# Kernel optimization log

Hardware: AMD Instinct MI355X
Metric: run time of the kernel (lower is better)

Reference implementation:

```python
import jax, jax.numpy as jnp
import numpy as np

DEPTH = 4  # truncation depth of the tensor algebra


def _tprod(a, b):
    # tensor (outer) product of level-i and level-j terms, flattened row-major
    # a: (B, C^i), b: (B, C^j) -> (B, C^(i+j))
    return (a[:, :, None] * b[:, None, :]).reshape(a.shape[0], -1)


def _exp_levels(dx):
    # exp(dx) in the truncated tensor algebra: level k = dx^{\otimes k} / k!
    levels = [dx]
    for k in range(2, DEPTH + 1):
        levels.append(_tprod(levels[-1], dx) / k)
    return tuple(levels)


def _chen(a, b):
    # Chen's identity: (a \otimes b)_k = a_k + b_k + sum_{i=1}^{k-1} a_i \otimes b_{k-i}
    out = []
    for k in range(1, DEPTH + 1):
        t = a[k - 1] + b[k - 1]
        for i in range(1, k):
            t = t + _tprod(a[i - 1], b[k - 1 - i])
        out.append(t)
    return tuple(out)


def _log_levels(s):
    # log(1 + x) = sum_{n>=1} (-1)^{n+1}/n x^{\otimes n}, x = S - 1 (levels 1..DEPTH)
    res = list(s)
    power = [t for t in s]  # x^{\otimes 1}; entries may become None (structurally zero)
    for n in range(2, DEPTH + 1):
        new = [None] * DEPTH
        for k in range(n, DEPTH + 1):
            acc = None
            for i in range(n - 1, k):
                if power[i - 1] is None:
                    continue
                term = _tprod(power[i - 1], s[k - i - 1])
                acc = term if acc is None else acc + term
            new[k - 1] = acc
        power = new
        coef = ((-1.0) ** (n + 1)) / n
        for k in range(n, DEPTH + 1):
            if power[k - 1] is not None:
                res[k - 1] = res[k - 1] + coef * power[k - 1]
    return tuple(res)


def _logsignature(path):
    # path: (B, L, C); no basepoint, stream=False, inverse=False, mode='expand'
    dxs = jnp.moveaxis(path[:, 1:] - path[:, :-1], 1, 0)  # (L-1, B, C)
    init = _exp_levels(dxs[0])

    def step(carry, dx):
        return _chen(carry, _exp_levels(dx)), None

    sig, _ = jax.lax.scan(step, init, dxs[1:])
    logsig = _log_levels(sig)
    return jnp.concatenate(logsig, axis=-1)  # (B, C + C^2 + ... + C^DEPTH)


def setup_inputs() -> dict:
    key = jax.random.key(0)
    # scale so high tensor-algebra levels stay well-conditioned in fp32
    path = 0.1 * jax.random.normal(key, (64, 256, 16), dtype=jnp.float32)
    return {"path": path}


def reference(path):
    return _logsignature(path)
```

## Files before the change

### kernel.cpp

```cpp
#include <hip/hip_runtime.h>


#define NC 16
#define NL 256
#define NB 64
#define NSTEP 255
#define OUTB 69904
#define SIG123 4368
#define OFF_L2 16
#define OFF_L3 272
#define OFF_L4 4368

#define SIGA_OFF 0
#define SIGB_OFF (NB * SIG123)
#define B4_OFF (2 * NB * SIG123)

__global__ __launch_bounds__(256, 4) void k_scan(const float* __restrict__ path,
                                                 float* __restrict__ out,
                                                 float* __restrict__ b4,
                                                 float* __restrict__ sigA,
                                                 float* __restrict__ sigB) {
    const int bid = blockIdx.x;
    const int j = bid >> 4;
    const int a = bid & 15;
    const int tid = threadIdx.x;
    const int h = tid >> 7;
    const int b = (tid >> 3) & 15;
    const int c0 = tid & 7;

    __shared__ float Lp[NL * NC];
    __shared__ float Ld[NSTEP * NC];

    const float* pj = path + (size_t)j * NL * NC;
#pragma unroll
    for (int k = 0; k < 4; ++k) {
        const int f = tid + k * 256;
        *(float4*)&Lp[f * 4] = *(const float4*)&pj[f * 4];
    }
    __syncthreads();

#pragma unroll
    for (int k = 0; k < 4; ++k) {
        const int f = tid + k * 256;
        if (f < 1020) {
            const float4 x0 = *(const float4*)&Lp[f * 4];
            const float4 x1 = *(const float4*)&Lp[f * 4 + 16];
            *(float4*)&Ld[f * 4] =
                make_float4(x1.x - x0.x, x1.y - x0.y, x1.z - x0.z, x1.w - x0.w);
        }
    }
    __syncthreads();

    float s4a[16], s4b[16];
#pragma unroll
    for (int d = 0; d < 16; ++d) { s4a[d] = 0.f; s4b[d] = 0.f; }
    float s3_0 = 0.f, s3_1 = 0.f, s2ab = 0.f, s1a = 0.f;

    const int t0 = h ? 128 : 0;
    const int t1 = h ? NSTEP : 128;

    int t = t0;
    const int nv = (t1 - t0) >> 2;
    for (int it = 0; it < nv; ++it) {
#pragma unroll
        for (int u = 0; u < 4; ++u, ++t) {
            const float* r = Ld + t * NC;
            const float4 q0 = *(const float4*)(r);
            const float4 q1 = *(const float4*)(r + 4);
            const float4 q2 = *(const float4*)(r + 8);
            const float4 q3 = *(const float4*)(r + 12);
            const float dxa = r[a];
            const float dxb = r[b];
            const float dxc0 = r[c0];
            const float dxc1 = r[c0 + 8];

            const float P = dxb * s1a;
            const float Q = dxb * dxa;
            const float pre4 = fmaf(1.f / 6.f, P, fmaf(1.f / 24.f, Q, 0.5f * s2ab));
            const float U = fmaf(0.5f, P, fmaf(1.f / 6.f, Q, s2ab));
            const float T0 = fmaf(dxc0, pre4, s3_0);
            const float T1 = fmaf(dxc1, pre4, s3_1);
            const float dv[16] = {q0.x, q0.y, q0.z, q0.w, q1.x, q1.y, q1.z, q1.w,
                                  q2.x, q2.y, q2.z, q2.w, q3.x, q3.y, q3.z, q3.w};
#pragma unroll
            for (int d = 0; d < 16; ++d) {
                s4a[d] = fmaf(dv[d], T0, s4a[d]);
                s4b[d] = fmaf(dv[d], T1, s4b[d]);
            }
            s3_0 = fmaf(dxc0, U, s3_0);
            s3_1 = fmaf(dxc1, U, s3_1);
            s2ab = fmaf(dxb, fmaf(0.5f, dxa, s1a), s2ab);
            s1a += dxa;
        }
    }
    for (; t < t1; ++t) {
        const float* r = Ld + t * NC;
        const float4 q0 = *(const float4*)(r);
        const float4 q1 = *(const float4*)(r + 4);
        const float4 q2 = *(const float4*)(r + 8);
        const float4 q3 = *(const float4*)(r + 12);
        const float dxa = r[a];
        const float dxb = r[b];
        const float dxc0 = r[c0];
        const float dxc1 = r[c0 + 8];
        const float P = dxb * s1a;
        const float Q = dxb * dxa;
        const float pre4 = fmaf(1.f / 6.f, P, fmaf(1.f / 24.f, Q, 0.5f * s2ab));
        const float U = fmaf(0.5f, P, fmaf(1.f / 6.f, Q, s2ab));
        const float T0 = fmaf(dxc0, pre4, s3_0);
        const float T1 = fmaf(dxc1, pre4, s3_1);
        const float dv[16] = {q0.x, q0.y, q0.z, q0.w, q1.x, q1.y, q1.z, q1.w,
                              q2.x, q2.y, q2.z, q2.w, q3.x, q3.y, q3.z, q3.w};
#pragma unroll
        for (int d = 0; d < 16; ++d) {
            s4a[d] = fmaf(dv[d], T0, s4a[d]);
            s4b[d] = fmaf(dv[d], T1, s4b[d]);
        }
        s3_0 = fmaf(dxc0, U, s3_0);
        s3_1 = fmaf(dxc1, U, s3_1);
        s2ab = fmaf(dxb, fmaf(0.5f, dxa, s1a), s2ab);
        s1a += dxa;
    }

    __syncthreads();
    float* ls = Lp;

    if (h == 0) {
        const int base = b * 256 + c0 * 16;
#pragma unroll
        for (int d = 0; d < 16; d += 4) {
            *(float4*)&ls[base + d] = make_float4(s4a[d], s4a[d + 1], s4a[d + 2], s4a[d + 3]);
            *(float4*)&ls[base + 128 + d] =
                make_float4(s4b[d], s4b[d + 1], s4b[d + 2], s4b[d + 3]);
        }
    }
    __syncthreads();
    {
        float* o4 = out + (size_t)j * OUTB + OFF_L4 + a * 4096;
#pragma unroll
        for (int k = 0; k < 4; ++k) {
            const int f = tid + k * 256;
            *(float4*)(o4 + f * 4) = *(const float4*)&ls[f * 4];
        }
    }
    __syncthreads();

    if (h == 1) {
        const int base = b * 256 + c0 * 16;
#pragma unroll
        for (int d = 0; d < 16; d += 4) {
            *(float4*)&ls[base + d] = make_float4(s4a[d], s4a[d + 1], s4a[d + 2], s4a[d + 3]);
            *(float4*)&ls[base + 128 + d] =
                make_float4(s4b[d], s4b[d + 1], s4b[d + 2], s4b[d + 3]);
        }
    }
    __syncthreads();
    {
        float* o4 = b4 + (((size_t)j * 16 + a) << 12);
#pragma unroll
        for (int k = 0; k < 4; ++k) {
            const int f = tid + k * 256;
            *(float4*)(o4 + f * 4) = *(const float4*)&ls[f * 4];
        }
    }

    float* sg = (h ? sigB : sigA) + (size_t)j * SIG123;
    sg[OFF_L3 + (a * 16 + b) * 16 + c0] = s3_0;
    sg[OFF_L3 + (a * 16 + b) * 16 + c0 + 8] = s3_1;
    if (c0 == 0) sg[OFF_L2 + a * 16 + b] = s2ab;
    if ((tid & 127) == 0) sg[a] = s1a;
}

__global__ __launch_bounds__(256) void k_log(const float* __restrict__ sigA,
                                             const float* __restrict__ sigB,
                                             const float* __restrict__ b4,
                                             float* __restrict__ out) {
    const int bid = blockIdx.x;
    const int j = bid >> 4;
    const int a = bid & 15;
    const int tid = threadIdx.x;
    const int q = tid >> 4;
    const int r = tid & 15;

    const float* A = sigA + (size_t)j * SIG123;
    const float* Bp = sigB + (size_t)j * SIG123;

    __shared__ float S1m[16], B1s[16], A2s[16];
    __shared__ float S2m[256], B2s[256], A3s[256];
    __shared__ float S3m[4096], B3s[4096];

    const float b1r = Bp[r];
    const float b2t = Bp[OFF_L2 + tid];

    if (tid < 16) {
        const float bb = Bp[tid];
        B1s[tid] = bb;
        S1m[tid] = A[tid] + bb;
        A2s[tid] = A[OFF_L2 + a * 16 + tid];
    }
    B2s[tid] = b2t;
    S2m[tid] = A[OFF_L2 + tid] + b2t + A[q] * b1r;
    A3s[tid] = A[OFF_L3 + a * 256 + tid];
#pragma unroll
    for (int k = 0; k < 16; ++k) {
        const int m = k * 256 + tid;
        const float b3 = Bp[OFF_L3 + m];
        B3s[m] = b3;
        S3m[m] = A[OFF_L3 + m] + b3 + A[k] * b2t + A[OFF_L2 + k * 16 + q] * b1r;
    }
    __syncthreads();

    const float s1a = S1m[a];
    const float A1a = A[a];
    float* outj = out + (size_t)j * OUTB;
    float* o4 = outj + OFF_L4 + a * 4096;
    const float* B4 = b4 + (((size_t)j * 16 + a) << 12);
    const float Ac = -0.5f * s1a;

#pragma unroll
    for (int k = 0; k < 4; ++k) {
        const int f = tid + k * 256;
        const int m0 = f * 4;
        const int bb = m0 >> 8;
        const int cc = (m0 >> 4) & 15;
        const float s1b = S1m[bb], s1c = S1m[cc];
        const float s2ab = S2m[a * 16 + bb];
        const float s2bc = S2m[bb * 16 + cc];
        const float s3abc = S3m[a * 256 + (m0 >> 4)];
        const float a3x = A3s[m0 >> 4];
        const float a2x = A2s[bb];

        const float4 a4 = *(const float4*)(o4 + m0);
        const float4 b4v = *(const float4*)(B4 + m0);
        const float4 b3v = *(const float4*)(&B3s[m0]);
        const float4 b2v = *(const float4*)(&B2s[m0 & 255]);
        const float4 b1v = *(const float4*)(&B1s[m0 & 15]);
        const float4 v3 = *(const float4*)(&S3m[m0]);
        const float4 v2 = *(const float4*)(&S2m[m0 & 255]);
        const float4 v1 = *(const float4*)(&S1m[m0 & 15]);

        const float Bv = fmaf((1.f / 3.f) * s1a, s1b, -0.5f * s2ab);
        const float Cv = -0.5f * s3abc + (1.f / 3.f) * fmaf(s1a, s2bc, s2ab * s1c)
                         - 0.25f * s1a * s1b * s1c;
        float4 rr;
        rr.x = a4.x + b4v.x + fmaf(A1a, b3v.x, fmaf(a2x, b2v.x, a3x * b1v.x));
        rr.y = a4.y + b4v.y + fmaf(A1a, b3v.y, fmaf(a2x, b2v.y, a3x * b1v.y));
        rr.z = a4.z + b4v.z + fmaf(A1a, b3v.z, fmaf(a2x, b2v.z, a3x * b1v.z));
        rr.w = a4.w + b4v.w + fmaf(A1a, b3v.w, fmaf(a2x, b2v.w, a3x * b1v.w));
        rr.x = fmaf(Ac, v3.x, rr.x) + fmaf(Bv, v2.x, Cv * v1.x);
        rr.y = fmaf(Ac, v3.y, rr.y) + fmaf(Bv, v2.y, Cv * v1.y);
        rr.z = fmaf(Ac, v3.z, rr.z) + fmaf(Bv, v2.z, Cv * v1.z);
        rr.w = fmaf(Ac, v3.w, rr.w) + fmaf(Bv, v2.w, Cv * v1.w);
        *(float4*)(o4 + m0) = rr;
    }

    {
        const float s1b = S1m[q], s1c = S1m[r];
        const float s2ab = S2m[a * 16 + q];
        const float s2bc = S2m[q * 16 + r];
        const float s3abc = S3m[a * 256 + tid];
        const float r3 = s3abc - 0.5f * fmaf(s1a, s2bc, s2ab * s1c)
                         + (1.f / 3.f) * s1a * s1b * s1c;
        outj[OFF_L3 + a * 256 + tid] = r3;
    }
    if (tid < 16) outj[OFF_L2 + a * 16 + tid] = fmaf(-0.5f * s1a, S1m[tid], S2m[a * 16 + tid]);
    if (tid == 0) outj[a] = s1a;
}

extern "C" void kernel_launch(void* const* d_in, const int* in_sizes, int n_in,
                              void* d_out, int out_size, void* d_ws, size_t ws_size,
                              hipStream_t stream) {
    const float* path = (const float*)d_in[0];
    float* out = (float*)d_out;
    float* ws = (float*)d_ws;
    float* sigA = ws + SIGA_OFF;
    float* sigB = ws + SIGB_OFF;
    float* b4 = ws + B4_OFF;

    k_scan<<<NB * 16, 256, 0, stream>>>(path, out, b4, sigA, sigB);
    k_log<<<NB * 16, 256, 0, stream>>>(sigA, sigB, b4, out);
}
```

Before: 113.3 us.

## Merge half-scan level-4 sums in LDS and transpose increments for vector loads

The level-4 partial sums of the two half-scans are now added in shared memory before a single global write, which removes the b4 workspace buffer and its extra global write and read in the log kernel. Path increments are also stored in a channel-major transposed LDS array, so each thread fetches its four scalar channels for four timesteps with one float4 load instead of scalar loads. The log kernel reads B level-3 directly from global memory instead of staging it in shared memory, which lowers LDS use. The cost is an extra barrier and a read-modify-write pass over LDS, plus global loads in the log kernel's inner loop.

After: 109.3 us. -3.5%, faster.

```diff
diff --git a/kernel.cpp b/kernel.cpp
--- a/kernel.cpp
+++ b/kernel.cpp
@@ -13,11 +13,11 @@
 
 #define SIGA_OFF 0
 #define SIGB_OFF (NB * SIG123)
-#define B4_OFF (2 * NB * SIG123)
+
+#define LCS 260
 
 __global__ __launch_bounds__(256, 4) void k_scan(const float* __restrict__ path,
                                                  float* __restrict__ out,
-                                                 float* __restrict__ b4,
                                                  float* __restrict__ sigA,
                                                  float* __restrict__ sigB) {
     const int bid = blockIdx.x;
@@ -29,7 +29,7 @@
     const int c0 = tid & 7;
 
     __shared__ float Lp[NL * NC];
-    __shared__ float Ld[NSTEP * NC];
+    __shared__ float Lc[NC * LCS];
 
     const float* pj = path + (size_t)j * NL * NC;
 #pragma unroll
@@ -39,14 +39,28 @@
     }
     __syncthreads();
 
+    float4 dif[4];
 #pragma unroll
     for (int k = 0; k < 4; ++k) {
         const int f = tid + k * 256;
         if (f < 1020) {
             const float4 x0 = *(const float4*)&Lp[f * 4];
             const float4 x1 = *(const float4*)&Lp[f * 4 + 16];
-            *(float4*)&Ld[f * 4] =
-                make_float4(x1.x - x0.x, x1.y - x0.y, x1.z - x0.z, x1.w - x0.w);
+            dif[k] = make_float4(x1.x - x0.x, x1.y - x0.y, x1.z - x0.z, x1.w - x0.w);
+        }
+    }
+    __syncthreads();
+#pragma unroll
+    for (int k = 0; k < 4; ++k) {
+        const int f = tid + k * 256;
+        if (f < 1020) {
+            *(float4*)&Lp[f * 4] = dif[k];
+            const int t = f >> 2;
+            const int i0 = 4 * (f & 3);
+            Lc[(i0 + 0) * LCS + t] = dif[k].x;
+            Lc[(i0 + 1) * LCS + t] = dif[k].y;
+            Lc[(i0 + 2) * LCS + t] = dif[k].z;
+            Lc[(i0 + 3) * LCS + t] = dif[k].w;
         }
     }
     __syncthreads();
@@ -61,18 +75,22 @@
 
     int t = t0;
     const int nv = (t1 - t0) >> 2;
-    for (int it = 0; it < nv; ++it) {
-#pragma unroll
-        for (int u = 0; u < 4; ++u, ++t) {
-            const float* r = Ld + t * NC;
+    for (int it = 0; it < nv; ++it, t += 4) {
+        const float4 va = *(const float4*)(Lc + a * LCS + t);
+        const float4 vb = *(const float4*)(Lc + b * LCS + t);
+        const float4 vc0 = *(const float4*)(Lc + c0 * LCS + t);
+        const float4 vc1 = *(const float4*)(Lc + (c0 + 8) * LCS + t);
+#pragma unroll
+        for (int u = 0; u < 4; ++u) {
+            const float* r = Lp + (t + u) * NC;
             const float4 q0 = *(const float4*)(r);
             const float4 q1 = *(const float4*)(r + 4);
             const float4 q2 = *(const float4*)(r + 8);
             const float4 q3 = *(const float4*)(r + 12);
-            const float dxa = r[a];
-            const float dxb = r[b];
-            const float dxc0 = r[c0];
-            const float dxc1 = r[c0 + 8];
+            const float dxa = (u == 0) ? va.x : (u == 1) ? va.y : (u == 2) ? va.z : va.w;
+            const float dxb = (u == 0) ? vb.x : (u == 1) ? vb.y : (u == 2) ? vb.z : vb.w;
+            const float dxc0 = (u == 0) ? vc0.x : (u == 1) ? vc0.y : (u == 2) ? vc0.z : vc0.w;
+            const float dxc1 = (u == 0) ? vc1.x : (u == 1) ? vc1.y : (u == 2) ? vc1.z : vc1.w;
 
             const float P = dxb * s1a;
             const float Q = dxb * dxa;
@@ -94,7 +112,7 @@
         }
     }
     for (; t < t1; ++t) {
-        const float* r = Ld + t * NC;
+        const float* r = Lp + t * NC;
         const float4 q0 = *(const float4*)(r);
         const float4 q1 = *(const float4*)(r + 4);
         const float4 q2 = *(const float4*)(r + 8);
@@ -124,9 +142,8 @@
 
     __syncthreads();
     float* ls = Lp;
-
+    const int base = b * 256 + c0 * 16;
     if (h == 0) {
-        const int base = b * 256 + c0 * 16;
 #pragma unroll
         for (int d = 0; d < 16; d += 4) {
             *(float4*)&ls[base + d] = make_float4(s4a[d], s4a[d + 1], s4a[d + 2], s4a[d + 3]);
@@ -135,28 +152,20 @@
         }
     }
     __syncthreads();
+    if (h == 1) {
+#pragma unroll
+        for (int d = 0; d < 16; d += 4) {
+            float4 v0 = *(const float4*)&ls[base + d];
+            v0.x += s4a[d]; v0.y += s4a[d + 1]; v0.z += s4a[d + 2]; v0.w += s4a[d + 3];
+            *(float4*)&ls[base + d] = v0;
+            float4 v1 = *(const float4*)&ls[base + 128 + d];
+            v1.x += s4b[d]; v1.y += s4b[d + 1]; v1.z += s4b[d + 2]; v1.w += s4b[d + 3];
+            *(float4*)&ls[base + 128 + d] = v1;
+        }
+    }
+    __syncthreads();
     {
         float* o4 = out + (size_t)j * OUTB + OFF_L4 + a * 4096;
-#pragma unroll
-        for (int k = 0; k < 4; ++k) {
-            const int f = tid + k * 256;
-            *(float4*)(o4 + f * 4) = *(const float4*)&ls[f * 4];
-        }
-    }
-    __syncthreads();
-
-    if (h == 1) {
-        const int base = b * 256 + c0 * 16;
-#pragma unroll
-        for (int d = 0; d < 16; d += 4) {
-            *(float4*)&ls[base + d] = make_float4(s4a[d], s4a[d + 1], s4a[d + 2], s4a[d + 3]);
-            *(float4*)&ls[base + 128 + d] =
-                make_float4(s4b[d], s4b[d + 1], s4b[d + 2], s4b[d + 3]);
-        }
-    }
-    __syncthreads();
-    {
-        float* o4 = b4 + (((size_t)j * 16 + a) << 12);
 #pragma unroll
         for (int k = 0; k < 4; ++k) {
             const int f = tid + k * 256;
@@ -173,7 +182,6 @@
 
 __global__ __launch_bounds__(256) void k_log(const float* __restrict__ sigA,
                                              const float* __restrict__ sigB,
-                                             const float* __restrict__ b4,
                                              float* __restrict__ out) {
     const int bid = blockIdx.x;
     const int j = bid >> 4;
@@ -187,7 +195,7 @@
 
     __shared__ float S1m[16], B1s[16], A2s[16];
     __shared__ float S2m[256], B2s[256], A3s[256];
-    __shared__ float S3m[4096], B3s[4096];
+    __shared__ float S3m[4096];
 
     const float b1r = Bp[r];
     const float b2t = Bp[OFF_L2 + tid];
@@ -204,9 +212,7 @@
 #pragma unroll
     for (int k = 0; k < 16; ++k) {
         const int m = k * 256 + tid;
-        const float b3 = Bp[OFF_L3 + m];
-        B3s[m] = b3;
-        S3m[m] = A[OFF_L3 + m] + b3 + A[k] * b2t + A[OFF_L2 + k * 16 + q] * b1r;
+        S3m[m] = A[OFF_L3 + m] + Bp[OFF_L3 + m] + A[k] * b2t + A[OFF_L2 + k * 16 + q] * b1r;
     }
     __syncthreads();
 
@@ -214,7 +220,6 @@
     const float A1a = A[a];
     float* outj = out + (size_t)j * OUTB;
     float* o4 = outj + OFF_L4 + a * 4096;
-    const float* B4 = b4 + (((size_t)j * 16 + a) << 12);
     const float Ac = -0.5f * s1a;
 
 #pragma unroll
@@ -231,8 +236,7 @@
         const float a2x = A2s[bb];
 
         const float4 a4 = *(const float4*)(o4 + m0);
-        const float4 b4v = *(const float4*)(B4 + m0);
-        const float4 b3v = *(const float4*)(&B3s[m0]);
+        const float4 b3v = *(const float4*)(Bp + OFF_L3 + m0);
         const float4 b2v = *(const float4*)(&B2s[m0 & 255]);
         const float4 b1v = *(const float4*)(&B1s[m0 & 15]);
         const float4 v3 = *(const float4*)(&S3m[m0]);
@@ -243,10 +247,10 @@
         const float Cv = -0.5f * s3abc + (1.f / 3.f) * fmaf(s1a, s2bc, s2ab * s1c)
                          - 0.25f * s1a * s1b * s1c;
         float4 rr;
-        rr.x = a4.x + b4v.x + fmaf(A1a, b3v.x, fmaf(a2x, b2v.x, a3x * b1v.x));
-        rr.y = a4.y + b4v.y + fmaf(A1a, b3v.y, fmaf(a2x, b2v.y, a3x * b1v.y));
-        rr.z = a4.z + b4v.z + fmaf(A1a, b3v.z, fmaf(a2x, b2v.z, a3x * b1v.z));
-        rr.w = a4.w + b4v.w + fmaf(A1a, b3v.w, fmaf(a2x, b2v.w, a3x * b1v.w));
+        rr.x = a4.x + fmaf(A1a, b3v.x, fmaf(a2x, b2v.x, a3x * b1v.x));
+        rr.y = a4.y + fmaf(A1a, b3v.y, fmaf(a2x, b2v.y, a3x * b1v.y));
+        rr.z = a4.z + fmaf(A1a, b3v.z, fmaf(a2x, b2v.z, a3x * b1v.z));
+        rr.w = a4.w + fmaf(A1a, b3v.w, fmaf(a2x, b2v.w, a3x * b1v.w));
         rr.x = fmaf(Ac, v3.x, rr.x) + fmaf(Bv, v2.x, Cv * v1.x);
         rr.y = fmaf(Ac, v3.y, rr.y) + fmaf(Bv, v2.y, Cv * v1.y);
         rr.z = fmaf(Ac, v3.z, rr.z) + fmaf(Bv, v2.z, Cv * v1.z);
@@ -275,8 +279,7 @@
     float* ws = (float*)d_ws;
     float* sigA = ws + SIGA_OFF;
     float* sigB = ws + SIGB_OFF;
-    float* b4 = ws + B4_OFF;
-
-    k_scan<<<NB * 16, 256, 0, stream>>>(path, out, b4, sigA, sigB);
-    k_log<<<NB * 16, 256, 0, stream>>>(sigA, sigB, b4, out);
+
+    k_scan<<<NB * 16, 256, 0, stream>>>(path, out, sigA, sigB);
+    k_log<<<NB * 16, 256, 0, stream>>>(sigA, sigB, out);
 }
```
